# Kernel tuning notes

Measured on AMD Instinct MI355X. Metric: run time of the kernel, lower is better.

The kernel has to match this reference:

```python
import jax, jax.numpy as jnp
import numpy as np


def setup_inputs() -> dict:
    key = jax.random.key(0)
    k1, k2 = jax.random.split(key)
    B, L1, L2, D = 8, 2048, 2048, 128
    seq_1 = jax.random.normal(k1, (B, L1, D), dtype=jnp.float32)
    seq_2 = jax.random.normal(k2, (B, L2, D), dtype=jnp.float32)
    return {"seq_1": seq_1, "seq_2": seq_2}


def reference(seq_1, seq_2):
    # e_ij: [B, L1, L2] cross-attention scores
    e_ij = jnp.einsum("bid,bjd->bij", seq_1, seq_2)
    # softmax over seq_2 positions (axis=2) to attend into seq_2
    w2 = jax.nn.softmax(e_ij, axis=2)
    # softmax over seq_1 positions (axis=1) to attend into seq_1
    w1 = jax.nn.softmax(e_ij, axis=1)
    seq_1_hat = jnp.einsum("bij,bjd->bid", w2, seq_2)  # [B, L1, D]
    seq_2_hat = jnp.einsum("bij,bid->bjd", w1, seq_1)  # [B, L2, D]
    return (seq_1_hat, seq_2_hat)
```

## Files before the change

kernel.cpp:

```cpp
#include <hip/hip_runtime.h>
#include <hip/hip_bf16.h>
#include <math.h>


#define LSEQ 2048
#define DIM  128
#define NBATCH 8
#define BM 128
#define BJ 128
#define NJT (LSEQ / BJ)
#define THR_DEFER 8.0f
#define PLANE (NBATCH * LSEQ * DIM)

typedef _Float16 halfT;
typedef halfT v8h  __attribute__((ext_vector_type(8)));
typedef float v16f __attribute__((ext_vector_type(16)));
typedef float v4f  __attribute__((ext_vector_type(4)));
typedef unsigned v4u __attribute__((ext_vector_type(4)));

__device__ __forceinline__ unsigned pk2u(float a, float b) {
    auto p = __builtin_amdgcn_cvt_pkrtz(a, b);
    return __builtin_bit_cast(unsigned, p);
}

__device__ __forceinline__ void gload16(const void* g, void* l) {
    __builtin_amdgcn_global_load_lds(
        (const __attribute__((address_space(1))) unsigned int*)g,
        (__attribute__((address_space(3))) unsigned int*)l, 16, 0, 0);
}

__device__ __forceinline__ v16f vz16() {
    v16f z;
    #pragma unroll
    for (int r = 0; r < 16; ++r) z[r] = 0.f;
    return z;
}

__global__ __launch_bounds__(256, 4)
void prepass_kernel(const float* __restrict__ S1, const float* __restrict__ S2,
                    short* __restrict__ ws)
{
    __shared__ short Th[DIM][66];
    const int lt = blockIdx.x;
    const int bb = blockIdx.y;
    const int tn = blockIdx.z;
    const float* src = (tn ? S2 : S1) + ((size_t)bb * LSEQ + (size_t)lt * 64) * DIM;
    short* hi = ws + (size_t)tn * 2 * PLANE + ((size_t)bb * LSEQ + (size_t)lt * 64) * DIM;
    short* tr = ws + (size_t)tn * 2 * PLANE + (size_t)PLANE
              + (size_t)bb * DIM * LSEQ + (size_t)lt * 64;
    const int tid = threadIdx.x;
    #pragma unroll
    for (int it = 0; it < 8; ++it) {
        int idx = tid + it * 256;
        int r = idx >> 5;
        int c = (idx & 31) * 4;
        float4 v = *(const float4*)(src + (size_t)r * DIM + c);
        halfT h0 = (halfT)v.x, h1 = (halfT)v.y, h2 = (halfT)v.z, h3 = (halfT)v.w;
        short b0 = __builtin_bit_cast(short, h0), b1 = __builtin_bit_cast(short, h1);
        short b2 = __builtin_bit_cast(short, h2), b3 = __builtin_bit_cast(short, h3);
        *(short4*)&hi[(size_t)r * DIM + c] = make_short4(b0, b1, b2, b3);
        Th[c + 0][r] = b0; Th[c + 1][r] = b1;
        Th[c + 2][r] = b2; Th[c + 3][r] = b3;
    }
    __syncthreads();
    #pragma unroll
    for (int it = 0; it < 16; ++it) {
        int idx = tid + it * 256;
        int d = idx >> 5;
        int c = (idx & 31) * 2;
        unsigned val = (unsigned)(unsigned short)Th[d][c]
                     | ((unsigned)(unsigned short)Th[d][c + 1] << 16);
        *(unsigned*)(tr + (size_t)d * LSEQ + c) = val;
    }
}

__global__ __launch_bounds__(1024, 1)
void xattn_main(const short* __restrict__ ws, float* __restrict__ out)
{
    __shared__ char pool[131072];
    __shared__ float mEx[4][4][32], sEx[4][4][32], facM[4][4][32];

    const int tid  = threadIdx.x;
    const int lane = tid & 63;
    const int wave = tid >> 6;
    const int wv   = wave & 3;
    const int wq   = wave >> 2;
    const int li   = lane & 31;
    const int h    = lane >> 5;
    const int swz  = (li & 15) << 4;

    const int bx   = blockIdx.x;
    const int xcd  = bx & 7;
    const int slot = bx >> 3;
    const int g    = xcd * 2 + (slot >> 4);
    const int rt   = slot & 15;
    const int side = g >> 3;
    const int bb   = g & 7;

    const short* XHg = ws + (size_t)side * 2 * PLANE + ((size_t)bb * LSEQ + (size_t)rt * BM) * DIM;
    const short* YHg = ws + (size_t)(side ^ 1) * 2 * PLANE + (size_t)bb * LSEQ * DIM;
    const short* YTg = ws + (size_t)(side ^ 1) * 2 * PLANE + (size_t)PLANE + (size_t)bb * DIM * LSEQ;
    float* O = out + (size_t)side * PLANE + ((size_t)bb * LSEQ + (size_t)rt * BM) * DIM;

    float runm = -INFINITY, runs = 0.f;

    const int ch0 = wave * 2;
    const int sr0 = ch0 * 4 + (lane >> 4);
    const int sr1 = (ch0 + 1) * 4 + (lane >> 4);
    const int sc0 = ((lane & 15) * 16) ^ ((sr0 & 15) << 4);
    const int sc1 = ((lane & 15) * 16) ^ ((sr1 & 15) << 4);

    auto STAGE_Y = [&](int jt) {
        gload16((const char*)YHg + ((size_t)(jt * BJ + sr0)) * 256 + sc0,
                pool + ch0 * 1024);
        gload16((const char*)YHg + ((size_t)(jt * BJ + sr1)) * 256 + sc1,
                pool + (ch0 + 1) * 1024);
    };
    auto STAGE_V = [&](int jt, int b) {
        gload16((const char*)YTg + (size_t)sr0 * (LSEQ * 2) + (size_t)jt * (BJ * 2) + sc0,
                pool + 32768 + b * 32768 + ch0 * 1024);
        gload16((const char*)YTg + (size_t)sr1 * (LSEQ * 2) + (size_t)jt * (BJ * 2) + sc1,
                pool + 32768 + b * 32768 + (ch0 + 1) * 1024);
    };

    v16f o0 = vz16(), o1 = vz16(), o2 = vz16(), o3 = vz16();

    gload16((const char*)XHg + (size_t)sr0 * 256 + sc0, pool + 98304 + ch0 * 1024);
    gload16((const char*)XHg + (size_t)sr1 * 256 + sc1, pool + 98304 + (ch0 + 1) * 1024);
    STAGE_Y(0);
    STAGE_V(0, 0);
    asm volatile("s_waitcnt vmcnt(0)" ::: "memory");
    __syncthreads();

    const int yrow = wq * 32 + li;
    const int xrow = wv * 32 + li;

    for (int jt = 0; jt < NJT; ++jt) {
        const int cur = jt & 1;

        v16f e = vz16();
        __builtin_amdgcn_s_setprio(1);
        #pragma unroll
        for (int ks = 0; ks < 8; ++ks) {
            const int cb = ks * 32 + h * 16;
            v8h ya = *(const v8h*)(pool + yrow * 256 + (cb ^ ((yrow & 15) << 4)));
            v8h xv = *(const v8h*)(pool + 98304 + xrow * 256 + (cb ^ ((xrow & 15) << 4)));
            e = __builtin_amdgcn_mfma_f32_32x32x16_f16(ya, xv, e, 0, 0, 0);
        }
        __builtin_amdgcn_s_setprio(0);

        asm volatile("s_waitcnt lgkmcnt(0)" ::: "memory");
        __builtin_amdgcn_s_barrier();
        __builtin_amdgcn_sched_barrier(0);

        if (jt + 1 < NJT) {
            STAGE_Y(jt + 1);
            STAGE_V(jt + 1, cur ^ 1);
        }

        float a0 = fmaxf(e[0], e[1]),  a1 = fmaxf(e[2], e[3]);
        float a2 = fmaxf(e[4], e[5]),  a3 = fmaxf(e[6], e[7]);
        float a4 = fmaxf(e[8], e[9]),  a5 = fmaxf(e[10], e[11]);
        float a6 = fmaxf(e[12], e[13]), a7 = fmaxf(e[14], e[15]);
        float mt = fmaxf(fmaxf(fmaxf(a0, a1), fmaxf(a2, a3)),
                         fmaxf(fmaxf(a4, a5), fmaxf(a6, a7)));
        mt = fmaxf(mt, __shfl_xor(mt, 32));

        float f = 1.0f;
        if (mt > runm + THR_DEFER) { f = __expf(runm - mt); runm = mt; runs *= f; }

        float s = 0.f;
        #pragma unroll
        for (int r = 0; r < 16; ++r) { e[r] = __expf(e[r] - runm); s += e[r]; }
        s += __shfl_xor(s, 32);
        runs += s;

        if (__any(f != 1.0f)) {
            #pragma unroll
            for (int r = 0; r < 16; ++r) {
                const float fr = __shfl(f, (r & 3) + 8 * (r >> 2) + 4 * h);
                o0[r] *= fr; o1[r] *= fr; o2[r] *= fr; o3[r] *= fr;
            }
        }

        const char* Vc = pool + 32768 + cur * 32768;
        __builtin_amdgcn_s_setprio(1);
        #pragma unroll
        for (int ks2 = 0; ks2 < 2; ++ks2) {
            const int base = ks2 * 8;
            unsigned kA0 = pk2u(e[base + 0], e[base + 1]);
            unsigned kA1 = pk2u(e[base + 2], e[base + 3]);
            unsigned kB0 = pk2u(e[base + 4], e[base + 5]);
            unsigned kB1 = pk2u(e[base + 6], e[base + 7]);
            unsigned r0 = (unsigned)__shfl_xor((int)(h ? kA0 : kB0), 32);
            unsigned r1 = (unsigned)__shfl_xor((int)(h ? kA1 : kB1), 32);
            v4u U;
            U[0] = h ? r0 : kA0;
            U[1] = h ? r1 : kA1;
            U[2] = h ? kB0 : r0;
            U[3] = h ? kB1 : r1;
            v8h pa = __builtin_bit_cast(v8h, U);
            const int cj = wq * 64 + ks2 * 32 + h * 16;
            v8h vb0 = *(const v8h*)(Vc + (0 * 32 + li) * 256 + (cj ^ ((li & 15) << 4)));
            v8h vb1 = *(const v8h*)(Vc + (1 * 32 + li) * 256 + (cj ^ ((li & 15) << 4)));
            v8h vb2 = *(const v8h*)(Vc + (2 * 32 + li) * 256 + (cj ^ ((li & 15) << 4)));
            v8h vb3 = *(const v8h*)(Vc + (3 * 32 + li) * 256 + (cj ^ ((li & 15) << 4)));
            o0 = __builtin_amdgcn_mfma_f32_32x32x16_f16(pa, vb0, o0, 0, 0, 0);
            o1 = __builtin_amdgcn_mfma_f32_32x32x16_f16(pa, vb1, o1, 0, 0, 0);
            o2 = __builtin_amdgcn_mfma_f32_32x32x16_f16(pa, vb2, o2, 0, 0, 0);
            o3 = __builtin_amdgcn_mfma_f32_32x32x16_f16(pa, vb3, o3, 0, 0, 0);
        }
        __builtin_amdgcn_s_setprio(0);

        asm volatile("s_waitcnt vmcnt(0) lgkmcnt(0)" ::: "memory");
        __builtin_amdgcn_s_barrier();
        __builtin_amdgcn_sched_barrier(0);
    }

    if (lane < 32) { mEx[wv][wq][lane] = runm; sEx[wv][wq][lane] = runs; }
    __syncthreads();
    if (tid < 128) {
        const int wv2 = tid >> 5, li2 = tid & 31;
        float m0 = mEx[wv2][0][li2], m1 = mEx[wv2][1][li2];
        float m2 = mEx[wv2][2][li2], m3 = mEx[wv2][3][li2];
        float mM = fmaxf(fmaxf(m0, m1), fmaxf(m2, m3));
        float e0 = __expf(m0 - mM), e1 = __expf(m1 - mM);
        float e2 = __expf(m2 - mM), e3 = __expf(m3 - mM);
        float inv = 1.0f / (sEx[wv2][0][li2] * e0 + sEx[wv2][1][li2] * e1 +
                            sEx[wv2][2][li2] * e2 + sEx[wv2][3][li2] * e3);
        facM[wv2][0][li2] = e0 * inv;
        facM[wv2][1][li2] = e1 * inv;
        facM[wv2][2][li2] = e2 * inv;
        facM[wv2][3][li2] = e3 * inv;
    }
    __syncthreads();
    #pragma unroll
    for (int r = 0; r < 16; ++r) {
        const float fr = facM[wv][wq][(r & 3) + 8 * (r >> 2) + 4 * h];
        o0[r] *= fr; o1[r] *= fr; o2[r] *= fr; o3[r] *= fr;
    }

    auto obWrite = [&](char* basep) {
        #pragma unroll
        for (int rg = 0; rg < 4; ++rg) {
            const int chs = ((wv * 8 + rg * 2 + h) ^ li) << 4;
            *(v4f*)(basep + (0 * 32 + li) * 512 + chs) =
                (v4f){o0[rg * 4 + 0], o0[rg * 4 + 1], o0[rg * 4 + 2], o0[rg * 4 + 3]};
            *(v4f*)(basep + (1 * 32 + li) * 512 + chs) =
                (v4f){o1[rg * 4 + 0], o1[rg * 4 + 1], o1[rg * 4 + 2], o1[rg * 4 + 3]};
            *(v4f*)(basep + (2 * 32 + li) * 512 + chs) =
                (v4f){o2[rg * 4 + 0], o2[rg * 4 + 1], o2[rg * 4 + 2], o2[rg * 4 + 3]};
            *(v4f*)(basep + (3 * 32 + li) * 512 + chs) =
                (v4f){o3[rg * 4 + 0], o3[rg * 4 + 1], o3[rg * 4 + 2], o3[rg * 4 + 3]};
        }
    };
    auto obAdd = [&](const char* basep) {
        #pragma unroll
        for (int rg = 0; rg < 4; ++rg) {
            const int chs = ((wv * 8 + rg * 2 + h) ^ li) << 4;
            v4f v0 = *(const v4f*)(basep + (0 * 32 + li) * 512 + chs);
            v4f v1 = *(const v4f*)(basep + (1 * 32 + li) * 512 + chs);
            v4f v2 = *(const v4f*)(basep + (2 * 32 + li) * 512 + chs);
            v4f v3 = *(const v4f*)(basep + (3 * 32 + li) * 512 + chs);
            #pragma unroll
            for (int q = 0; q < 4; ++q) {
                o0[rg * 4 + q] += v0[q];
                o1[rg * 4 + q] += v1[q];
                o2[rg * 4 + q] += v2[q];
                o3[rg * 4 + q] += v3[q];
            }
        }
    };

    __syncthreads();
    if (wq == 1) obWrite(pool);
    if (wq == 3) obWrite(pool + 65536);
    __syncthreads();
    if (wq == 0) obAdd(pool);
    if (wq == 2) obAdd(pool + 65536);
    __syncthreads();
    if (wq == 2) obWrite(pool);
    __syncthreads();
    if (wq == 0) {
        obAdd(pool);
        #pragma unroll
        for (int r = 0; r < 16; ++r) {
            const int i = wv * 32 + (r & 3) + 8 * (r >> 2) + 4 * h;
            float* orow = O + (size_t)i * DIM;
            orow[0 * 32 + li] = o0[r];
            orow[1 * 32 + li] = o1[r];
            orow[2 * 32 + li] = o2[r];
            orow[3 * 32 + li] = o3[r];
        }
    }
}

extern "C" void kernel_launch(void* const* d_in, const int* in_sizes, int n_in,
                              void* d_out, int out_size, void* d_ws, size_t ws_size,
                              hipStream_t stream) {
    const float* s1 = (const float*)d_in[0];
    const float* s2 = (const float*)d_in[1];
    float* out = (float*)d_out;
    short* ws = (short*)d_ws;
    prepass_kernel<<<dim3(LSEQ / 64, NBATCH, 2), 256, 0, stream>>>(s1, s2, ws);
    xattn_main<<<dim3(256), 1024, 0, stream>>>(ws, out);
}
```

Measured before the change: 71.15 us.

## Share row max across waves and split PV by output columns instead of key blocks

Each wave now shares its per-row tile max through LDS, so all four key-column waves use a common running max. The probability tile is written to LDS and the PV product is split by output D columns rather than key chunks. This removes the final cross-wave reduction of four full accumulators, cuts accumulator registers from four tiles to one, and keeps the X operand in registers instead of LDS. In exchange it adds an extra barrier and LDS round trips for the P tile and the max exchange on every iteration.

```diff
diff --git a/kernel.cpp b/kernel.cpp
--- a/kernel.cpp
+++ b/kernel.cpp
@@ -15,8 +15,6 @@
 typedef _Float16 halfT;
 typedef halfT v8h  __attribute__((ext_vector_type(8)));
 typedef float v16f __attribute__((ext_vector_type(16)));
-typedef float v4f  __attribute__((ext_vector_type(4)));
-typedef unsigned v4u __attribute__((ext_vector_type(4)));
 
 __device__ __forceinline__ unsigned pk2u(float a, float b) {
     auto p = __builtin_amdgcn_cvt_pkrtz(a, b);
@@ -78,16 +76,17 @@
 void xattn_main(const short* __restrict__ ws, float* __restrict__ out)
 {
     __shared__ char pool[131072];
-    __shared__ float mEx[4][4][32], sEx[4][4][32], facM[4][4][32];
+    __shared__ float maxp[4][4][32];
+    __shared__ float sEx[4][4][32];
 
     const int tid  = threadIdx.x;
     const int lane = tid & 63;
     const int wave = tid >> 6;
-    const int wv   = wave & 3;
-    const int wq   = wave >> 2;
+    const int wA   = wave & 3;
+    const int wB   = wave >> 2;
     const int li   = lane & 31;
     const int h    = lane >> 5;
-    const int swz  = (li & 15) << 4;
+    const int sl   = (li & 15) << 4;
 
     const int bx   = blockIdx.x;
     const int xcd  = bx & 7;
@@ -102,7 +101,16 @@
     const short* YTg = ws + (size_t)(side ^ 1) * 2 * PLANE + (size_t)PLANE + (size_t)bb * DIM * LSEQ;
     float* O = out + (size_t)side * PLANE + ((size_t)bb * LSEQ + (size_t)rt * BM) * DIM;
 
+    v8h xv[8];
+    {
+        const short* xr = XHg + (size_t)(wA * 32 + li) * DIM + h * 8;
+        #pragma unroll
+        for (int ks = 0; ks < 8; ++ks)
+            xv[ks] = *(const v8h*)(const void*)(xr + ks * 16);
+    }
+
     float runm = -INFINITY, runs = 0.f;
+    v16f o = vz16();
 
     const int ch0 = wave * 2;
     const int sr0 = ch0 * 4 + (lane >> 4);
@@ -123,17 +131,15 @@
                 pool + 32768 + b * 32768 + (ch0 + 1) * 1024);
     };
 
-    v16f o0 = vz16(), o1 = vz16(), o2 = vz16(), o3 = vz16();
-
-    gload16((const char*)XHg + (size_t)sr0 * 256 + sc0, pool + 98304 + ch0 * 1024);
-    gload16((const char*)XHg + (size_t)sr1 * 256 + sc1, pool + 98304 + (ch0 + 1) * 1024);
     STAGE_Y(0);
     STAGE_V(0, 0);
     asm volatile("s_waitcnt vmcnt(0)" ::: "memory");
     __syncthreads();
 
-    const int yrow = wq * 32 + li;
-    const int xrow = wv * 32 + li;
+    const int yrow = wB * 32 + li;
+    const int prow = wA * 32 + li;
+    const int vrow = wB * 32 + li;
+    char* PtB = pool + 98304;
 
     for (int jt = 0; jt < NJT; ++jt) {
         const int cur = jt & 1;
@@ -142,12 +148,18 @@
         __builtin_amdgcn_s_setprio(1);
         #pragma unroll
         for (int ks = 0; ks < 8; ++ks) {
-            const int cb = ks * 32 + h * 16;
-            v8h ya = *(const v8h*)(pool + yrow * 256 + (cb ^ ((yrow & 15) << 4)));
-            v8h xv = *(const v8h*)(pool + 98304 + xrow * 256 + (cb ^ ((xrow & 15) << 4)));
-            e = __builtin_amdgcn_mfma_f32_32x32x16_f16(ya, xv, e, 0, 0, 0);
+            v8h ya = *(const v8h*)(pool + yrow * 256 + ((ks * 32 + h * 16) ^ sl));
+            e = __builtin_amdgcn_mfma_f32_32x32x16_f16(ya, xv[ks], e, 0, 0, 0);
         }
         __builtin_amdgcn_s_setprio(0);
+
+        float a0 = fmaxf(fmaxf(e[0], e[1]),  fmaxf(e[2], e[3]));
+        float a1 = fmaxf(fmaxf(e[4], e[5]),  fmaxf(e[6], e[7]));
+        float a2 = fmaxf(fmaxf(e[8], e[9]),  fmaxf(e[10], e[11]));
+        float a3 = fmaxf(fmaxf(e[12], e[13]), fmaxf(e[14], e[15]));
+        float mt = fmaxf(fmaxf(a0, a1), fmaxf(a2, a3));
+        mt = fmaxf(mt, __shfl_xor(mt, 32));
+        if (lane < 32) maxp[wA][wB][lane] = mt;
 
         asm volatile("s_waitcnt lgkmcnt(0)" ::: "memory");
         __builtin_amdgcn_s_barrier();
@@ -158,16 +170,10 @@
             STAGE_V(jt + 1, cur ^ 1);
         }
 
-        float a0 = fmaxf(e[0], e[1]),  a1 = fmaxf(e[2], e[3]);
-        float a2 = fmaxf(e[4], e[5]),  a3 = fmaxf(e[6], e[7]);
-        float a4 = fmaxf(e[8], e[9]),  a5 = fmaxf(e[10], e[11]);
-        float a6 = fmaxf(e[12], e[13]), a7 = fmaxf(e[14], e[15]);
-        float mt = fmaxf(fmaxf(fmaxf(a0, a1), fmaxf(a2, a3)),
-                         fmaxf(fmaxf(a4, a5), fmaxf(a6, a7)));
-        mt = fmaxf(mt, __shfl_xor(mt, 32));
-
+        float m4 = fmaxf(fmaxf(maxp[wA][0][li], maxp[wA][1][li]),
+                         fmaxf(maxp[wA][2][li], maxp[wA][3][li]));
         float f = 1.0f;
-        if (mt > runm + THR_DEFER) { f = __expf(runm - mt); runm = mt; runs *= f; }
+        if (m4 > runm + THR_DEFER) { f = __expf(runm - m4); runs *= f; runm = m4; }
 
         float s = 0.f;
         #pragma unroll
@@ -177,38 +183,30 @@
 
         if (__any(f != 1.0f)) {
             #pragma unroll
-            for (int r = 0; r < 16; ++r) {
-                const float fr = __shfl(f, (r & 3) + 8 * (r >> 2) + 4 * h);
-                o0[r] *= fr; o1[r] *= fr; o2[r] *= fr; o3[r] *= fr;
-            }
-        }
+            for (int r = 0; r < 16; ++r)
+                o[r] *= __shfl(f, (r & 3) + 8 * (r >> 2) + 4 * h);
+        }
+
+        #pragma unroll
+        for (int gq = 0; gq < 4; ++gq) {
+            unsigned u0 = pk2u(e[gq * 4 + 0], e[gq * 4 + 1]);
+            unsigned u1 = pk2u(e[gq * 4 + 2], e[gq * 4 + 3]);
+            unsigned long long uu = (unsigned long long)u0 | ((unsigned long long)u1 << 32);
+            const int gran = (wB * 4 + gq) ^ (li & 15);
+            *(unsigned long long*)(PtB + prow * 256 + gran * 16 + h * 8) = uu;
+        }
+
+        asm volatile("s_waitcnt lgkmcnt(0)" ::: "memory");
+        __builtin_amdgcn_s_barrier();
+        __builtin_amdgcn_sched_barrier(0);
 
         const char* Vc = pool + 32768 + cur * 32768;
         __builtin_amdgcn_s_setprio(1);
         #pragma unroll
-        for (int ks2 = 0; ks2 < 2; ++ks2) {
-            const int base = ks2 * 8;
-            unsigned kA0 = pk2u(e[base + 0], e[base + 1]);
-            unsigned kA1 = pk2u(e[base + 2], e[base + 3]);
-            unsigned kB0 = pk2u(e[base + 4], e[base + 5]);
-            unsigned kB1 = pk2u(e[base + 6], e[base + 7]);
-            unsigned r0 = (unsigned)__shfl_xor((int)(h ? kA0 : kB0), 32);
-            unsigned r1 = (unsigned)__shfl_xor((int)(h ? kA1 : kB1), 32);
-            v4u U;
-            U[0] = h ? r0 : kA0;
-            U[1] = h ? r1 : kA1;
-            U[2] = h ? kB0 : r0;
-            U[3] = h ? kB1 : r1;
-            v8h pa = __builtin_bit_cast(v8h, U);
-            const int cj = wq * 64 + ks2 * 32 + h * 16;
-            v8h vb0 = *(const v8h*)(Vc + (0 * 32 + li) * 256 + (cj ^ ((li & 15) << 4)));
-            v8h vb1 = *(const v8h*)(Vc + (1 * 32 + li) * 256 + (cj ^ ((li & 15) << 4)));
-            v8h vb2 = *(const v8h*)(Vc + (2 * 32 + li) * 256 + (cj ^ ((li & 15) << 4)));
-            v8h vb3 = *(const v8h*)(Vc + (3 * 32 + li) * 256 + (cj ^ ((li & 15) << 4)));
-            o0 = __builtin_amdgcn_mfma_f32_32x32x16_f16(pa, vb0, o0, 0, 0, 0);
-            o1 = __builtin_amdgcn_mfma_f32_32x32x16_f16(pa, vb1, o1, 0, 0, 0);
-            o2 = __builtin_amdgcn_mfma_f32_32x32x16_f16(pa, vb2, o2, 0, 0, 0);
-            o3 = __builtin_amdgcn_mfma_f32_32x32x16_f16(pa, vb3, o3, 0, 0, 0);
+        for (int ks = 0; ks < 8; ++ks) {
+            v8h pa = *(const v8h*)(PtB + prow * 256 + (((ks * 2 + h) ^ (li & 15)) << 4));
+            v8h vb = *(const v8h*)(Vc + vrow * 256 + ((ks * 32 + h * 16) ^ sl));
+            o = __builtin_amdgcn_mfma_f32_32x32x16_f16(pa, vb, o, 0, 0, 0);
         }
         __builtin_amdgcn_s_setprio(0);
 
@@ -217,81 +215,15 @@
         __builtin_amdgcn_sched_barrier(0);
     }
 
-    if (lane < 32) { mEx[wv][wq][lane] = runm; sEx[wv][wq][lane] = runs; }
+    if (lane < 32) sEx[wA][wB][lane] = runs;
     __syncthreads();
-    if (tid < 128) {
-        const int wv2 = tid >> 5, li2 = tid & 31;
-        float m0 = mEx[wv2][0][li2], m1 = mEx[wv2][1][li2];
-        float m2 = mEx[wv2][2][li2], m3 = mEx[wv2][3][li2];
-        float mM = fmaxf(fmaxf(m0, m1), fmaxf(m2, m3));
-        float e0 = __expf(m0 - mM), e1 = __expf(m1 - mM);
-        float e2 = __expf(m2 - mM), e3 = __expf(m3 - mM);
-        float inv = 1.0f / (sEx[wv2][0][li2] * e0 + sEx[wv2][1][li2] * e1 +
-                            sEx[wv2][2][li2] * e2 + sEx[wv2][3][li2] * e3);
-        facM[wv2][0][li2] = e0 * inv;
-        facM[wv2][1][li2] = e1 * inv;
-        facM[wv2][2][li2] = e2 * inv;
-        facM[wv2][3][li2] = e3 * inv;
-    }
-    __syncthreads();
+    const float inv = 1.0f / ((sEx[wA][0][li] + sEx[wA][1][li]) +
+                              (sEx[wA][2][li] + sEx[wA][3][li]));
     #pragma unroll
     for (int r = 0; r < 16; ++r) {
-        const float fr = facM[wv][wq][(r & 3) + 8 * (r >> 2) + 4 * h];
-        o0[r] *= fr; o1[r] *= fr; o2[r] *= fr; o3[r] *= fr;
-    }
-
-    auto obWrite = [&](char* basep) {
-        #pragma unroll
-        for (int rg = 0; rg < 4; ++rg) {
-            const int chs = ((wv * 8 + rg * 2 + h) ^ li) << 4;
-            *(v4f*)(basep + (0 * 32 + li) * 512 + chs) =
-                (v4f){o0[rg * 4 + 0], o0[rg * 4 + 1], o0[rg * 4 + 2], o0[rg * 4 + 3]};
-            *(v4f*)(basep + (1 * 32 + li) * 512 + chs) =
-                (v4f){o1[rg * 4 + 0], o1[rg * 4 + 1], o1[rg * 4 + 2], o1[rg * 4 + 3]};
-            *(v4f*)(basep + (2 * 32 + li) * 512 + chs) =
-                (v4f){o2[rg * 4 + 0], o2[rg * 4 + 1], o2[rg * 4 + 2], o2[rg * 4 + 3]};
-            *(v4f*)(basep + (3 * 32 + li) * 512 + chs) =
-                (v4f){o3[rg * 4 + 0], o3[rg * 4 + 1], o3[rg * 4 + 2], o3[rg * 4 + 3]};
-        }
-    };
-    auto obAdd = [&](const char* basep) {
-        #pragma unroll
-        for (int rg = 0; rg < 4; ++rg) {
-            const int chs = ((wv * 8 + rg * 2 + h) ^ li) << 4;
-            v4f v0 = *(const v4f*)(basep + (0 * 32 + li) * 512 + chs);
-            v4f v1 = *(const v4f*)(basep + (1 * 32 + li) * 512 + chs);
-            v4f v2 = *(const v4f*)(basep + (2 * 32 + li) * 512 + chs);
-            v4f v3 = *(const v4f*)(basep + (3 * 32 + li) * 512 + chs);
-            #pragma unroll
-            for (int q = 0; q < 4; ++q) {
-                o0[rg * 4 + q] += v0[q];
-                o1[rg * 4 + q] += v1[q];
-                o2[rg * 4 + q] += v2[q];
-                o3[rg * 4 + q] += v3[q];
-            }
-        }
-    };
-
-    __syncthreads();
-    if (wq == 1) obWrite(pool);
-    if (wq == 3) obWrite(pool + 65536);
-    __syncthreads();
-    if (wq == 0) obAdd(pool);
-    if (wq == 2) obAdd(pool + 65536);
-    __syncthreads();
-    if (wq == 2) obWrite(pool);
-    __syncthreads();
-    if (wq == 0) {
-        obAdd(pool);
-        #pragma unroll
-        for (int r = 0; r < 16; ++r) {
-            const int i = wv * 32 + (r & 3) + 8 * (r >> 2) + 4 * h;
-            float* orow = O + (size_t)i * DIM;
-            orow[0 * 32 + li] = o0[r];
-            orow[1 * 32 + li] = o1[r];
-            orow[2 * 32 + li] = o2[r];
-            orow[3 * 32 + li] = o3[r];
-        }
+        const int i = (r & 3) + 8 * (r >> 2) + 4 * h;
+        const float fr = __shfl(inv, i);
+        O[(size_t)(wA * 32 + i) * DIM + wB * 32 + li] = o[r] * fr;
     }
 }
 
```

Result: faster. 68.81 us (-3.3%).
